# Kernel tuning notes

Hardware: AMD Instinct MI355X
Metric: run time of the kernel (lower is better)

## Reference

```python
import jax, jax.numpy as jnp
import numpy as np

N = 50000          # nodes
K = 16             # neighbors per node
E = N * K          # edges
C_IN = 64
C_OUT = 64
BN_EPS = 1e-5


def _batchnorm(h, gamma, beta):
    # training-mode BatchNorm1d over the edge dimension (biased variance, as torch)
    mean = jnp.mean(h, axis=0)
    var = jnp.mean((h - mean) ** 2, axis=0)
    return gamma * (h - mean) * jax.lax.rsqrt(var + BN_EPS) + beta


def setup_inputs() -> dict:
    key = jax.random.key(0)
    ks = jax.random.split(key, 8)
    x = jax.random.normal(ks[0], (N, C_IN), dtype=jnp.float32)
    # destinations: every node has exactly K incoming edges (avoids empty segments)
    dst = jnp.repeat(jnp.arange(N, dtype=jnp.int64), K)
    src = jax.random.randint(ks[1], (E,), 0, N, dtype=jnp.int64)
    edge_index = jnp.stack([src, dst], axis=0)
    s1 = 1.0 / np.sqrt(2 * C_IN)
    s2 = 1.0 / np.sqrt(C_OUT)
    params = {
        "W1": jax.random.uniform(ks[2], (2 * C_IN, C_OUT), jnp.float32, -s1, s1),
        "b1": jnp.zeros((C_OUT,), jnp.float32),
        "g1": jnp.ones((C_OUT,), jnp.float32),
        "be1": jnp.zeros((C_OUT,), jnp.float32),
        "W2": jax.random.uniform(ks[3], (C_OUT, C_OUT), jnp.float32, -s2, s2),
        "b2": jnp.zeros((C_OUT,), jnp.float32),
        "g2": jnp.ones((C_OUT,), jnp.float32),
        "be2": jnp.zeros((C_OUT,), jnp.float32),
        "W3": jax.random.uniform(ks[4], (C_OUT, C_OUT), jnp.float32, -s2, s2),
        "b3": jnp.zeros((C_OUT,), jnp.float32),
    }
    return {"x": x, "edge_index": edge_index, **params}


def reference(x, edge_index, W1, b1, g1, be1, W2, b2, g2, be2, W3, b3):
    src, dst = edge_index[0], edge_index[1]
    x_i = x[dst]                      # [E, C_in] destination (center) features
    x_j = x[src]                      # [E, C_in] source (neighbor) features
    h = jnp.concatenate([x_i, x_j - x_i], axis=-1)   # [E, 2*C_in]
    h = jax.nn.leaky_relu(_batchnorm(h @ W1 + b1, g1, be1))
    h = jax.nn.leaky_relu(_batchnorm(h @ W2 + b2, g2, be2))
    h = h @ W3 + b3                   # [E, C_out]
    out = jax.ops.segment_max(h, dst, num_segments=N)  # scatter-max per dst node
    res = x                           # identity residual (in_channels == out_channels)
    return jax.nn.leaky_relu(out + res)
```

## Files before the change

kernel.cpp:

```cpp
#include <hip/hip_runtime.h>
#include <hip/hip_fp16.h>

#define N_NODES 50000
#define KNN     16
#define NEDGE   (N_NODES*KNN)
#define NTILE2  (NEDGE/128)
#define NWT     (N_NODES/16)
#define NB2     1024
#define SLOPE   0.01f
#define EPS     1e-5f

typedef __attribute__((ext_vector_type(8))) _Float16 f16x8;
typedef __attribute__((ext_vector_type(4))) float f32x4;

__device__ __forceinline__ unsigned short f2h(float f){
  union{_Float16 h; unsigned short u;} v; v.h = (_Float16)f; return v.u;
}
__device__ __forceinline__ unsigned short h2u(_Float16 h){
  union{_Float16 h; unsigned short u;} v; v.h = h; return v.u;
}
__device__ __forceinline__ f32x4 MFMA(f16x8 a, f16x8 b, f32x4 c){
  return __builtin_amdgcn_mfma_f32_16x16x32_f16(a, b, c, 0, 0, 0);
}
__device__ __forceinline__ float lrelu(float v){ return v>=0.f ? v : SLOPE*v; }

__global__ __launch_bounds__(256) void kUV(const float* __restrict__ x,
    const float* __restrict__ W1, unsigned short* __restrict__ Ub,
    unsigned short* __restrict__ Vb)
{
  const int t = threadIdx.x, w = t>>6, l = t&63, lr = l&15, lg = l>>4;
  const int wt = blockIdx.x*4 + w;
  if (wt >= NWT) return;

  f16x8 wfr[16];
#pragma unroll
  for (int f=0;f<16;++f){
    const int ks = f>>2, nf = f&3;
    const int k0 = ks*32 + (lg<<3);
    const int col = nf*16 + lr;
    f16x8 r;
#pragma unroll
    for (int e=0;e<8;++e){
      float v = W1[(size_t)(k0+e)*64 + col];
      if (f < 8) v -= W1[(size_t)(k0+e+64)*64 + col];
      r[e] = (_Float16)v;
    }
    wfr[f] = r;
  }

  const int n0 = wt*16;
  const float* xr = x + (size_t)(n0+lr)*64 + lg*8;
  f16x8 a0, a1;
#pragma unroll
  for (int e=0;e<8;++e){ a0[e] = (_Float16)xr[e]; a1[e] = (_Float16)xr[32+e]; }

  f32x4 aU[4], aV[4];
#pragma unroll
  for (int nf=0;nf<4;++nf){
    aU[nf] = (f32x4){0,0,0,0};
    aU[nf] = MFMA(a0, wfr[nf],    aU[nf]);
    aU[nf] = MFMA(a1, wfr[4+nf],  aU[nf]);
    aV[nf] = (f32x4){0,0,0,0};
    aV[nf] = MFMA(a0, wfr[8+nf],  aV[nf]);
    aV[nf] = MFMA(a1, wfr[12+nf], aV[nf]);
  }
#pragma unroll
  for (int nf=0;nf<4;++nf)
#pragma unroll
    for (int r=0;r<4;++r){
      const size_t o = (size_t)(n0 + 4*lg + r)*64 + 16*nf + lr;
      Ub[o] = f2h(aU[nf][r]);
      Vb[o] = f2h(aV[nf][r]);
    }
}

#define LOADUV(U0,U1,V0,V1, nodeId, srcId)                               \
  {                                                                      \
    const unsigned short* Ur = Ub + (size_t)(nodeId)*64 + lg*8;          \
    const unsigned short* Vr = Vb + (size_t)(srcId)*64  + lg*8;          \
    U0 = *(const f16x8*)(Ur); U1 = *(const f16x8*)(Ur + 32);             \
    V0 = *(const f16x8*)(Vr); V1 = *(const f16x8*)(Vr + 32);             \
  }

__global__ __launch_bounds__(256,4) void kS1(const unsigned short* __restrict__ Ub,
    const unsigned short* __restrict__ Vb, const int* __restrict__ ei,
    const float* __restrict__ W2, const float* __restrict__ W3,
    unsigned short* __restrict__ wf, float* __restrict__ part)
{
  __shared__ float red[4][128];
  const int t = threadIdx.x, w = t>>6, l = t&63, lr = l&15, lg = l>>4;
  const int G = gridDim.x;

  if (blockIdx.x < 4){
    const int idx = blockIdx.x*256 + t;
    const float* W = (idx < 512) ? W2 : W3;
    const int fi = (idx & 511) >> 6;
    const int ll = idx & 63;
    const int ks = fi >> 2, nf = fi & 3;
    const int k0 = ks*32 + ((ll>>4)<<3);
    const int col = nf*16 + (ll&15);
    unsigned short* o = wf + (size_t)idx*8;
#pragma unroll
    for (int e=0;e<8;++e) o[e] = f2h(W[(size_t)(k0+e)*64 + col]);
  }

  float s[16], q[16];
#pragma unroll
  for (int k=0;k<16;++k){ s[k]=0.f; q[k]=0.f; }

#define ACCST(U0,U1,V0,V1)                                              \
  {                                                                     \
    const f16x8 z0 = U0 + V0, z1 = U1 + V1;                             \
    _Pragma("unroll")                                                   \
    for (int e=0;e<8;++e){ const float zf=(float)z0[e]; s[e]+=zf; q[e]=fmaf(zf,zf,q[e]); } \
    _Pragma("unroll")                                                   \
    for (int e=0;e<8;++e){ const float zf=(float)z1[e]; s[8+e]+=zf; q[8+e]=fmaf(zf,zf,q[8+e]); } \
  }

  int tile = blockIdx.x;
  int srcA = ei[tile*128 + (2*w)*16 + lr];
  int srcB = ei[tile*128 + (2*w+1)*16 + lr];
  for (; tile < NTILE2; tile += G){
    const int nA = tile*8 + 2*w, nB = nA + 1;
    f16x8 uA0,uA1,vA0,vA1, uB0,uB1,vB0,vB1;
    LOADUV(uA0,uA1,vA0,vA1, nA, srcA)
    LOADUV(uB0,uB1,vB0,vB1, nB, srcB)
    const int nt = tile + G;
    if (nt < NTILE2){
      srcA = ei[nt*128 + (2*w)*16 + lr];
      srcB = ei[nt*128 + (2*w+1)*16 + lr];
    }
    ACCST(uA0,uA1,vA0,vA1)
    ACCST(uB0,uB1,vB0,vB1)
  }

#pragma unroll
  for (int k=0;k<16;++k){
    float a=s[k]; a+=__shfl_xor(a,1,64); a+=__shfl_xor(a,2,64);
    a+=__shfl_xor(a,4,64); a+=__shfl_xor(a,8,64); s[k]=a;
    float b=q[k]; b+=__shfl_xor(b,1,64); b+=__shfl_xor(b,2,64);
    b+=__shfl_xor(b,4,64); b+=__shfl_xor(b,8,64); q[k]=b;
  }
  if (lr == 0){
#pragma unroll
    for (int e=0;e<8;++e){
      red[w][8*lg+e]    = s[e];
      red[w][32+8*lg+e] = s[8+e];
      red[w][64+8*lg+e] = q[e];
      red[w][96+8*lg+e] = q[8+e];
    }
  }
  __syncthreads();
  if (t < 128)
    part[(size_t)t*NB2 + blockIdx.x] = red[0][t]+red[1][t]+red[2][t]+red[3][t];
}

__global__ __launch_bounds__(256) void kFin(const float* __restrict__ part,
    const float* __restrict__ g, const float* __restrict__ be,
    float* __restrict__ coefs, unsigned short* __restrict__ coefsH, int nb)
{
  __shared__ float rs[256], rq[256];
  const int c = blockIdx.x, t = threadIdx.x;
  const float* ps = part + (size_t)c*nb;
  const float* pq = part + (size_t)(64+c)*nb;
  float s = 0.f, q = 0.f;
  for (int i=t; i<nb; i+=256){ s += ps[i]; q += pq[i]; }
  rs[t]=s; rq[t]=q;
  __syncthreads();
#pragma unroll
  for (int off=128; off>0; off>>=1){
    if (t < off){ rs[t]+=rs[t+off]; rq[t]+=rq[t+off]; }
    __syncthreads();
  }
  if (t==0){
    const float inv  = 1.0f/(float)NEDGE;
    const float mean = rs[0]*inv;
    const float var  = rq[0]*inv - mean*mean;
    const float a    = g[c]*rsqrtf(var + EPS);
    const float cc   = be[c] - mean*a;
    coefs[c]       = a;
    coefs[64 + c]  = cc;
    coefsH[c]      = f2h(a);
    coefsH[64 + c] = f2h(cc);
  }
}

#define LOAD_C1                                                         \
  f16x8 A1a, A1b, C1a, C1b;                                             \
  {                                                                     \
    const int kb = lg*8;                                                \
    A1a = *(const f16x8*)(coefsH1 + kb);                                \
    A1b = *(const f16x8*)(coefsH1 + 32 + kb);                           \
    C1a = *(const f16x8*)(coefsH1 + 64 + kb);                           \
    C1b = *(const f16x8*)(coefsH1 + 96 + kb);                           \
  }

#define H1F(h0f, h1f, U0,U1,V0,V1)                                      \
  f16x8 h0f, h1f;                                                       \
  {                                                                     \
    const f16x8 t0 = (U0 + V0) * A1a + C1a;                             \
    const f16x8 t1 = (U1 + V1) * A1b + C1b;                             \
    h0f = __builtin_elementwise_max(t0, t0 * (_Float16)0.01f);          \
    h1f = __builtin_elementwise_max(t1, t1 * (_Float16)0.01f);          \
  }

__global__ __launch_bounds__(256,4) void kS2(const unsigned short* __restrict__ Ub,
    const unsigned short* __restrict__ Vb, const int* __restrict__ ei,
    const uint4* __restrict__ wfg, const unsigned short* __restrict__ coefsH1,
    float* __restrict__ part)
{
  __shared__ uint4 wlds[512];
  __shared__ float red[4][128];
  const int t = threadIdx.x, w = t>>6, l = t&63, lr = l&15, lg = l>>4;
  const int G = gridDim.x;
  const f32x4 Z4 = (f32x4){0.f,0.f,0.f,0.f};

  for (int i=t; i<512; i+=256) wlds[i] = wfg[i];
  __syncthreads();
  LOAD_C1

  float sumP[4] = {0,0,0,0}, sqP[4] = {0,0,0,0};

  int tile = blockIdx.x;
  int srcA = ei[tile*128 + (2*w)*16 + lr];
  int srcB = ei[tile*128 + (2*w+1)*16 + lr];
  for (; tile < NTILE2; tile += G){
    const int nA = tile*8 + 2*w, nB = nA + 1;
    f16x8 uA0,uA1,vA0,vA1, uB0,uB1,vB0,vB1;
    LOADUV(uA0,uA1,vA0,vA1, nA, srcA)
    LOADUV(uB0,uB1,vB0,vB1, nB, srcB)
    const int nt = tile + G;
    if (nt < NTILE2){
      srcA = ei[nt*128 + (2*w)*16 + lr];
      srcB = ei[nt*128 + (2*w+1)*16 + lr];
    }

    H1F(hA0, hA1, uA0,uA1,vA0,vA1)
    H1F(hB0, hB1, uB0,uB1,vB0,vB1)

    f32x4 aA[4], aB[4];
#pragma unroll
    for (int nf=0;nf<4;++nf){
      union{uint4 v; f16x8 h;}q0, q1;
      q0.v = wlds[nf*64 + l];  q1.v = wlds[(4+nf)*64 + l];
      aA[nf] = MFMA(hA0, q0.h, Z4);  aA[nf] = MFMA(hA1, q1.h, aA[nf]);
      aB[nf] = MFMA(hB0, q0.h, Z4);  aB[nf] = MFMA(hB1, q1.h, aB[nf]);
    }
#pragma unroll
    for (int nf=0;nf<4;++nf)
#pragma unroll
      for (int r=0;r<4;++r){
        const float v0 = aA[nf][r], v1 = aB[nf][r];
        sumP[nf] += v0 + v1;
        sqP[nf] = fmaf(v0,v0,sqP[nf]);
        sqP[nf] = fmaf(v1,v1,sqP[nf]);
      }
  }

#pragma unroll
  for (int nf=0;nf<4;++nf){
    float s = sumP[nf], q = sqP[nf];
    s += __shfl_xor(s,16,64); s += __shfl_xor(s,32,64);
    q += __shfl_xor(q,16,64); q += __shfl_xor(q,32,64);
    if (l < 16){ red[w][nf*16+l] = s; red[w][64+nf*16+l] = q; }
  }
  __syncthreads();
  if (t < 128)
    part[(size_t)t*NB2 + blockIdx.x] = red[0][t]+red[1][t]+red[2][t]+red[3][t];
}

__global__ __launch_bounds__(256,4) void kS3(const unsigned short* __restrict__ Ub,
    const unsigned short* __restrict__ Vb, const int* __restrict__ ei,
    const uint4* __restrict__ wfg, const unsigned short* __restrict__ coefsH1,
    const float* __restrict__ coefs2, const float* __restrict__ b3,
    const float* __restrict__ x, float* __restrict__ out)
{
  __shared__ uint4 wlds[1024];
  __shared__ __align__(16) unsigned short buf[8][16][72];
  const int t = threadIdx.x, w = t>>6, l = t&63, lr = l&15, lg = l>>4;
  const int G = gridDim.x;
  const f32x4 Z4 = (f32x4){0.f,0.f,0.f,0.f};

  for (int i=t; i<1024; i+=256) wlds[i] = wfg[i];
  __syncthreads();
  LOAD_C1

  float a2v[4], c2v[4], bb[4];
#pragma unroll
  for (int nf=0;nf<4;++nf){
    a2v[nf]=coefs2[nf*16+lr]; c2v[nf]=coefs2[64+nf*16+lr];
    bb[nf] = b3[nf*16+lr];
  }

  int tile = blockIdx.x;
  int srcA = ei[tile*128 + (2*w)*16 + lr];
  int srcB = ei[tile*128 + (2*w+1)*16 + lr];
  for (; tile < NTILE2; tile += G){
    const int nA = tile*8 + 2*w, nB = nA + 1;
    f16x8 uA0,uA1,vA0,vA1, uB0,uB1,vB0,vB1;
    LOADUV(uA0,uA1,vA0,vA1, nA, srcA)
    LOADUV(uB0,uB1,vB0,vB1, nB, srcB)
    const int nt = tile + G;
    if (nt < NTILE2){
      srcA = ei[nt*128 + (2*w)*16 + lr];
      srcB = ei[nt*128 + (2*w+1)*16 + lr];
    }

    H1F(hA0, hA1, uA0,uA1,vA0,vA1)
    H1F(hB0, hB1, uB0,uB1,vB0,vB1)

    f32x4 aA[4], aB[4];
#pragma unroll
    for (int nf=0;nf<4;++nf){
      union{uint4 v; f16x8 h;}q0, q1;
      q0.v = wlds[nf*64 + l];  q1.v = wlds[(4+nf)*64 + l];
      aA[nf] = MFMA(hA0, q0.h, Z4);  aA[nf] = MFMA(hA1, q1.h, aA[nf]);
      aB[nf] = MFMA(hB0, q0.h, Z4);  aB[nf] = MFMA(hB1, q1.h, aB[nf]);
    }
#pragma unroll
    for (int nf=0;nf<4;++nf)
#pragma unroll
      for (int r=0;r<4;++r){
        buf[2*w  ][4*lg+r][16*nf+lr] = h2u((_Float16)lrelu(fmaf(a2v[nf], aA[nf][r], c2v[nf])));
        buf[2*w+1][4*lg+r][16*nf+lr] = h2u((_Float16)lrelu(fmaf(a2v[nf], aB[nf][r], c2v[nf])));
      }
    const f16x8 gA0 = *(const f16x8*)&buf[2*w  ][lr][8*lg];
    const f16x8 gA1 = *(const f16x8*)&buf[2*w  ][lr][32+8*lg];
    const f16x8 gB0 = *(const f16x8*)&buf[2*w+1][lr][8*lg];
    const f16x8 gB1 = *(const f16x8*)&buf[2*w+1][lr][32+8*lg];

    f32x4 cA[4], cB[4];
#pragma unroll
    for (int nf=0;nf<4;++nf){
      union{uint4 v; f16x8 h;}q0, q1;
      q0.v = wlds[512 + nf*64 + l];  q1.v = wlds[512 + (4+nf)*64 + l];
      cA[nf] = MFMA(gA0, q0.h, Z4);  cA[nf] = MFMA(gA1, q1.h, cA[nf]);
      cB[nf] = MFMA(gB0, q0.h, Z4);  cB[nf] = MFMA(gB1, q1.h, cB[nf]);
    }

#pragma unroll
    for (int nf=0;nf<4;++nf){
      float mA = fmaxf(fmaxf(cA[nf][0],cA[nf][1]), fmaxf(cA[nf][2],cA[nf][3]));
      mA = fmaxf(mA, __shfl_xor(mA,16,64));
      mA = fmaxf(mA, __shfl_xor(mA,32,64));
      float mB = fmaxf(fmaxf(cB[nf][0],cB[nf][1]), fmaxf(cB[nf][2],cB[nf][3]));
      mB = fmaxf(mB, __shfl_xor(mB,16,64));
      mB = fmaxf(mB, __shfl_xor(mB,32,64));
      if (l < 16){
        const float xA = x[(size_t)nA*64 + nf*16 + l];
        out[(size_t)nA*64 + nf*16 + l] = lrelu(mA + bb[nf] + xA);
        const float xB = x[(size_t)nB*64 + nf*16 + l];
        out[(size_t)nB*64 + nf*16 + l] = lrelu(mB + bb[nf] + xB);
      }
    }
  }
}

extern "C" void kernel_launch(void* const* d_in, const int* in_sizes, int n_in,
                              void* d_out, int out_size, void* d_ws, size_t ws_size,
                              hipStream_t stream) {
  const float* x   = (const float*)d_in[0];
  const int*   ei  = (const int*)d_in[1];
  const float* W1  = (const float*)d_in[2];
  const float* g1  = (const float*)d_in[4];
  const float* be1 = (const float*)d_in[5];
  const float* W2  = (const float*)d_in[6];
  const float* g2  = (const float*)d_in[8];
  const float* be2 = (const float*)d_in[9];
  const float* W3  = (const float*)d_in[10];
  const float* b3  = (const float*)d_in[11];
  float* out = (float*)d_out;

  float*          coefs  = (float*)d_ws;
  unsigned short* coefsH = (unsigned short*)((char*)d_ws + 1024);
  float*          part1  = (float*)((char*)d_ws + 2048);
  float*          part2  = part1 + (size_t)NB2*128;
  unsigned short* wfb    = (unsigned short*)((char*)part2 + (size_t)NB2*128*4);
  unsigned short* Ub     = (unsigned short*)((char*)wfb + 16384);
  unsigned short* Vb     = Ub + (size_t)N_NODES*64;

  kUV<<<(NWT+3)/4, 256, 0, stream>>>(x, W1, Ub, Vb);
  kS1<<<NB2, 256, 0, stream>>>(Ub, Vb, ei, W2, W3, wfb, part1);
  kFin<<<64, 256, 0, stream>>>(part1, g1, be1, coefs, coefsH, NB2);
  kS2<<<NB2, 256, 0, stream>>>(Ub, Vb, ei, (const uint4*)wfb, coefsH, part2);
  kFin<<<64, 256, 0, stream>>>(part2, g2, be2, coefs + 128, coefsH + 128, NB2);
  kS3<<<NB2, 256, 0, stream>>>(Ub, Vb, ei, (const uint4*)wfb, coefsH,
                               coefs + 128, b3, x, out);
}
```

Baseline: 99.14 us.

## Software-pipeline U/V gathers one tile ahead in all three edge kernels

Each of the three grid-stride edge kernels now loads the U/V feature rows for the next tile before computing on the current one, and prefetches source indices two tiles ahead. The aim is to hide gather latency behind the MFMA and reduction work. In exchange each lane holds a second set of eight f16x8 registers, which raises register pressure under launch_bounds(256,4). Out-of-range prefetches are clamped to index 0, so the last iteration issues a redundant load.

```diff
diff --git a/kernel.cpp b/kernel.cpp
--- a/kernel.cpp
+++ b/kernel.cpp
@@ -81,6 +81,40 @@
     U0 = *(const f16x8*)(Ur); U1 = *(const f16x8*)(Ur + 32);             \
     V0 = *(const f16x8*)(Vr); V1 = *(const f16x8*)(Vr + 32);             \
   }
+
+#define PIPE_PROLOGUE                                                    \
+  int tile = blockIdx.x;                                                 \
+  int sA = ei[tile*128 + (2*w)*16 + lr];                                 \
+  int sB = ei[tile*128 + (2*w+1)*16 + lr];                               \
+  f16x8 cuA0,cuA1,cvA0,cvA1, cuB0,cuB1,cvB0,cvB1;                        \
+  LOADUV(cuA0,cuA1,cvA0,cvA1, tile*8 + 2*w,     sA)                      \
+  LOADUV(cuB0,cuB1,cvB0,cvB1, tile*8 + 2*w + 1, sB)                      \
+  {                                                                      \
+    const int nt0 = tile + G;                                            \
+    if (nt0 < NTILE2){                                                   \
+      sA = ei[nt0*128 + (2*w)*16 + lr];                                  \
+      sB = ei[nt0*128 + (2*w+1)*16 + lr];                                \
+    } else { sA = 0; sB = 0; }                                           \
+  }
+
+#define PIPE_ISSUE_NEXT                                                  \
+  const int nt = tile + G;                                               \
+  const int nnA = (nt < NTILE2) ? nt*8 + 2*w : 0;                        \
+  const int nnB = (nt < NTILE2) ? nnA + 1 : 0;                           \
+  f16x8 nuA0,nuA1,nvA0,nvA1, nuB0,nuB1,nvB0,nvB1;                        \
+  LOADUV(nuA0,nuA1,nvA0,nvA1, nnA, sA)                                   \
+  LOADUV(nuB0,nuB1,nvB0,nvB1, nnB, sB)                                   \
+  {                                                                      \
+    const int nt2 = tile + 2*G;                                          \
+    if (nt2 < NTILE2){                                                   \
+      sA = ei[nt2*128 + (2*w)*16 + lr];                                  \
+      sB = ei[nt2*128 + (2*w+1)*16 + lr];                                \
+    } else { sA = 0; sB = 0; }                                           \
+  }
+
+#define PIPE_ROTATE                                                      \
+  cuA0=nuA0; cuA1=nuA1; cvA0=nvA0; cvA1=nvA1;                            \
+  cuB0=nuB0; cuB1=nuB1; cvB0=nvB0; cvB1=nvB1;
 
 __global__ __launch_bounds__(256,4) void kS1(const unsigned short* __restrict__ Ub,
     const unsigned short* __restrict__ Vb, const int* __restrict__ ei,
@@ -117,21 +151,12 @@
     for (int e=0;e<8;++e){ const float zf=(float)z1[e]; s[8+e]+=zf; q[8+e]=fmaf(zf,zf,q[8+e]); } \
   }
 
-  int tile = blockIdx.x;
-  int srcA = ei[tile*128 + (2*w)*16 + lr];
-  int srcB = ei[tile*128 + (2*w+1)*16 + lr];
+  PIPE_PROLOGUE
   for (; tile < NTILE2; tile += G){
-    const int nA = tile*8 + 2*w, nB = nA + 1;
-    f16x8 uA0,uA1,vA0,vA1, uB0,uB1,vB0,vB1;
-    LOADUV(uA0,uA1,vA0,vA1, nA, srcA)
-    LOADUV(uB0,uB1,vB0,vB1, nB, srcB)
-    const int nt = tile + G;
-    if (nt < NTILE2){
-      srcA = ei[nt*128 + (2*w)*16 + lr];
-      srcB = ei[nt*128 + (2*w+1)*16 + lr];
-    }
-    ACCST(uA0,uA1,vA0,vA1)
-    ACCST(uB0,uB1,vB0,vB1)
+    PIPE_ISSUE_NEXT
+    ACCST(cuA0,cuA1,cvA0,cvA1)
+    ACCST(cuB0,cuB1,cvB0,cvB1)
+    PIPE_ROTATE
   }
 
 #pragma unroll
@@ -221,22 +246,12 @@
 
   float sumP[4] = {0,0,0,0}, sqP[4] = {0,0,0,0};
 
-  int tile = blockIdx.x;
-  int srcA = ei[tile*128 + (2*w)*16 + lr];
-  int srcB = ei[tile*128 + (2*w+1)*16 + lr];
+  PIPE_PROLOGUE
   for (; tile < NTILE2; tile += G){
-    const int nA = tile*8 + 2*w, nB = nA + 1;
-    f16x8 uA0,uA1,vA0,vA1, uB0,uB1,vB0,vB1;
-    LOADUV(uA0,uA1,vA0,vA1, nA, srcA)
-    LOADUV(uB0,uB1,vB0,vB1, nB, srcB)
-    const int nt = tile + G;
-    if (nt < NTILE2){
-      srcA = ei[nt*128 + (2*w)*16 + lr];
-      srcB = ei[nt*128 + (2*w+1)*16 + lr];
-    }
-
-    H1F(hA0, hA1, uA0,uA1,vA0,vA1)
-    H1F(hB0, hB1, uB0,uB1,vB0,vB1)
+    PIPE_ISSUE_NEXT
+
+    H1F(hA0, hA1, cuA0,cuA1,cvA0,cvA1)
+    H1F(hB0, hB1, cuB0,cuB1,cvB0,cvB1)
 
     f32x4 aA[4], aB[4];
 #pragma unroll
@@ -255,6 +270,8 @@
         sqP[nf] = fmaf(v0,v0,sqP[nf]);
         sqP[nf] = fmaf(v1,v1,sqP[nf]);
       }
+
+    PIPE_ROTATE
   }
 
 #pragma unroll
@@ -292,22 +309,13 @@
     bb[nf] = b3[nf*16+lr];
   }
 
-  int tile = blockIdx.x;
-  int srcA = ei[tile*128 + (2*w)*16 + lr];
-  int srcB = ei[tile*128 + (2*w+1)*16 + lr];
+  PIPE_PROLOGUE
   for (; tile < NTILE2; tile += G){
     const int nA = tile*8 + 2*w, nB = nA + 1;
-    f16x8 uA0,uA1,vA0,vA1, uB0,uB1,vB0,vB1;
-    LOADUV(uA0,uA1,vA0,vA1, nA, srcA)
-    LOADUV(uB0,uB1,vB0,vB1, nB, srcB)
-    const int nt = tile + G;
-    if (nt < NTILE2){
-      srcA = ei[nt*128 + (2*w)*16 + lr];
-      srcB = ei[nt*128 + (2*w+1)*16 + lr];
-    }
-
-    H1F(hA0, hA1, uA0,uA1,vA0,vA1)
-    H1F(hB0, hB1, uB0,uB1,vB0,vB1)
+    PIPE_ISSUE_NEXT
+
+    H1F(hA0, hA1, cuA0,cuA1,cvA0,cvA1)
+    H1F(hB0, hB1, cuB0,cuB1,cvB0,cvB1)
 
     f32x4 aA[4], aB[4];
 #pragma unroll
@@ -353,6 +361,8 @@
         out[(size_t)nB*64 + nf*16 + l] = lrelu(mB + bb[nf] + xB);
       }
     }
+
+    PIPE_ROTATE
   }
 }
 
```

New measurement: 135.8 us. 1.37x slower.
